# Kernel tuning notes

Hardware: AMD Instinct MI355X
Metric: run time of the kernel (lower is better)

## Reference

```python
import jax, jax.numpy as jnp
import numpy as np

D_MODEL = 2048
N_HEADS = 16
D_HEAD = 128
ROPE_BASE = 10000.0


def _rope(q, k, start_pos):
    # q, k: [B, H, S, Dh]; standard rotate-half RoPE
    S, Dh = q.shape[-2], q.shape[-1]
    inv_freq = 1.0 / (ROPE_BASE ** (jnp.arange(0, Dh, 2, dtype=jnp.float32) / Dh))  # [Dh/2]
    pos = jnp.arange(S, dtype=jnp.float32) + start_pos                              # [S]
    ang = pos[:, None] * inv_freq[None, :]                                          # [S, Dh/2]
    cos = jnp.concatenate([jnp.cos(ang), jnp.cos(ang)], axis=-1)[None, None]        # [1,1,S,Dh]
    sin = jnp.concatenate([jnp.sin(ang), jnp.sin(ang)], axis=-1)[None, None]

    def rot_half(t):
        t1, t2 = jnp.split(t, 2, axis=-1)
        return jnp.concatenate([-t2, t1], axis=-1)

    return q * cos + rot_half(q) * sin, k * cos + rot_half(k) * sin


def setup_inputs() -> dict:
    key = jax.random.key(0)
    k1, k2, k3 = jax.random.split(key, 3)
    B, S = 2, 2048
    scale_in = 1.0 / np.sqrt(D_MODEL)
    x = jax.random.normal(k1, (B, S, D_MODEL), dtype=jnp.float32)
    w_qkv = jax.random.normal(k2, (3 * D_MODEL, D_MODEL), dtype=jnp.float32) * scale_in
    w_out = jax.random.normal(k3, (D_MODEL, D_MODEL), dtype=jnp.float32) * scale_in
    return {"x": x, "w_qkv": w_qkv, "w_out": w_out, "start_pos": 0}


def reference(x, w_qkv, w_out, start_pos):
    B, S, _ = x.shape
    scale = 1.0 / np.sqrt(D_HEAD)
    qkv = jnp.einsum('bsd,ed->bse', x, w_qkv)                 # [B,S,3D]
    q, k, v = jnp.split(qkv, 3, axis=-1)
    # [B,S,D] -> [B,H,S,Dh]
    reshape = lambda t: t.reshape(B, S, N_HEADS, D_HEAD).transpose(0, 2, 1, 3)
    q, k, v = reshape(q), reshape(k), reshape(v)
    q, k = _rope(q, k, start_pos)
    scores = jnp.einsum('bhqd,bhkd->bhqk', q, k) * scale      # [B,H,S,S]
    if S > 1:
        causal = jnp.tril(jnp.ones((S, S), dtype=bool))
        scores = jnp.where(causal[None, None], scores, -jnp.inf)
    attn = jax.nn.softmax(scores, axis=-1)
    out = jnp.einsum('bhqk,bhkd->bhqd', attn, v)              # [B,H,S,Dh]
    out = out.transpose(0, 2, 1, 3).reshape(B, S, D_MODEL)
    return jnp.einsum('bsd,ed->bse', out, w_out)
```

## Files before the change

kernel.cpp:

```cpp
#include <hip/hip_runtime.h>

typedef unsigned short ushort;
typedef __attribute__((ext_vector_type(8))) short short8;
typedef __attribute__((ext_vector_type(4))) float f32x4;

#define NH 16
#define DH 128
#define SEQ 2048
#define DMODEL 2048
#define GK 2048

__device__ __forceinline__ ushort f2bf(float f) {
  union { float f; unsigned u; } v; v.f = f;
  unsigned u = v.u;
  unsigned r = (u + 0x7fffu + ((u >> 16) & 1u)) >> 16;
  return (ushort)r;
}
__device__ __forceinline__ float bf2f(ushort h) {
  union { unsigned u; float f; } v; v.u = ((unsigned)h) << 16; return v.f;
}

__device__ __forceinline__ void async16(const ushort* g, ushort* l) {
  __builtin_amdgcn_global_load_lds(
      (const __attribute__((address_space(1))) unsigned*)g,
      (__attribute__((address_space(3))) unsigned*)l, 16, 0, 0);
}

__global__ void cast_kernel(const float* __restrict__ src, ushort* __restrict__ dst, int n4) {
  int i = blockIdx.x * blockDim.x + threadIdx.x;
  if (i >= n4) return;
  float4 v = ((const float4*)src)[i];
  unsigned long long p = (unsigned long long)f2bf(v.x)
                       | ((unsigned long long)f2bf(v.y) << 16)
                       | ((unsigned long long)f2bf(v.z) << 32)
                       | ((unsigned long long)f2bf(v.w) << 48);
  ((unsigned long long*)dst)[i] = p;
}

template<int MODE>
__global__ __launch_bounds__(256, 2)
void gemm_bt(const ushort* __restrict__ A, const ushort* __restrict__ B, int N,
             ushort* __restrict__ oq, ushort* __restrict__ ok, ushort* __restrict__ ov,
             float* __restrict__ of) {
  __shared__ ushort As[128 * 64];
  __shared__ ushort Bs[128 * 64];
  const int tid = threadIdx.x;
  const int lane = tid & 63;
  const int w = tid >> 6;
  const int wr = w >> 1, wc = w & 1;
  const int g = lane >> 4, l16 = lane & 15;
  const int m0 = blockIdx.y * 128;
  const int n0 = blockIdx.x * 128;

  f32x4 acc[4][4];
#pragma unroll
  for (int i = 0; i < 4; ++i)
#pragma unroll
    for (int j = 0; j < 4; ++j) acc[i][j] = (f32x4)0.f;

  const ushort* Ablk = A + (size_t)m0 * GK;
  const ushort* Bblk = B + (size_t)n0 * GK;

  for (int k0 = 0; k0 < GK; k0 += 64) {
#pragma unroll
    for (int it = 0; it < 4; ++it) {
      int e = (it * 256 + tid) * 8;
      int row = e >> 6, col = e & 63;
      async16(Ablk + (size_t)row * GK + k0 + col, &As[e]);
      async16(Bblk + (size_t)row * GK + k0 + col, &Bs[e]);
    }
    __syncthreads();
#pragma unroll
    for (int ks = 0; ks < 2; ++ks) {
      short8 af[4], bf[4];
#pragma unroll
      for (int mf = 0; mf < 4; ++mf)
        af[mf] = *(const short8*)&As[(wr * 64 + mf * 16 + l16) * 64 + ks * 32 + g * 8];
#pragma unroll
      for (int nf = 0; nf < 4; ++nf)
        bf[nf] = *(const short8*)&Bs[(wc * 64 + nf * 16 + l16) * 64 + ks * 32 + g * 8];
#pragma unroll
      for (int mf = 0; mf < 4; ++mf)
#pragma unroll
        for (int nf = 0; nf < 4; ++nf)
          acc[mf][nf] = __builtin_amdgcn_mfma_f32_16x16x32_bf16(af[mf], bf[nf], acc[mf][nf], 0, 0, 0);
    }
    __syncthreads();
  }

#pragma unroll
  for (int mf = 0; mf < 4; ++mf)
#pragma unroll
    for (int nf = 0; nf < 4; ++nf)
#pragma unroll
      for (int i = 0; i < 4; ++i) {
        int row = m0 + wr * 64 + mf * 16 + g * 4 + i;
        int col = n0 + wc * 64 + nf * 16 + l16;
        float val = acc[mf][nf][i];
        if (MODE == 0) {
          int which = col >> 11;
          int r = col & 2047;
          int h = r >> 7, dh = r & 127;
          int b = row >> 11, s = row & 2047;
          size_t dst = ((size_t)(b * NH + h) * SEQ + s) * DH + dh;
          ushort* o = (which == 0) ? oq : (which == 1 ? ok : ov);
          o[dst] = f2bf(val);
        } else {
          of[(size_t)row * N + col] = val;
        }
      }
}

__global__ void rope_kernel(ushort* __restrict__ q, ushort* __restrict__ k,
                            const int* __restrict__ spp) {
  int id = blockIdx.x * blockDim.x + threadIdx.x;
  int j = id & 63;
  int s = (id >> 6) & (SEQ - 1);
  int bh = id >> 17;
  size_t base = ((size_t)bh * SEQ + s) * DH;
  float pos = (float)(s + spp[0]);
  float ang = pos * __expf(-(float)j * (9.210340371976184f / 64.f));
  float c = cosf(ang), sn = sinf(ang);
  float q1 = bf2f(q[base + j]), q2 = bf2f(q[base + 64 + j]);
  q[base + j]      = f2bf(q1 * c - q2 * sn);
  q[base + 64 + j] = f2bf(q2 * c + q1 * sn);
  float k1 = bf2f(k[base + j]), k2 = bf2f(k[base + 64 + j]);
  k[base + j]      = f2bf(k1 * c - k2 * sn);
  k[base + 64 + j] = f2bf(k2 * c + k1 * sn);
}

__global__ __launch_bounds__(256, 2)
void attn_kernel(const ushort* __restrict__ Q, const ushort* __restrict__ K,
                 const ushort* __restrict__ V, ushort* __restrict__ O) {
  __shared__ ushort Ks[2][64 * 128];
  __shared__ ushort Vt[2][128 * 72];
  __shared__ ushort Ps[4][16 * 72];
  const int tid = threadIdx.x;
  const int lane = tid & 63;
  const int w = tid >> 6;
  const int g = lane >> 4, l16 = lane & 15;
  const int h = blockIdx.y, b = blockIdx.z;
  const int bh = b * NH + h;
  const ushort* Qb = Q + (size_t)bh * SEQ * DH;
  const ushort* Kb = K + (size_t)bh * SEQ * DH;
  const ushort* Vb = V + (size_t)bh * SEQ * DH;
  const float scale = 0.08838834764831845f;

  const int vkv = (tid >> 3) * 2;
  const int vd0 = (tid & 7) * 16;
  const int vmask = (tid & 7) << 3;

  for (int pass = 0; pass < 2; ++pass) {
    const int qt = pass == 0 ? (31 - (int)blockIdx.x) : (int)blockIdx.x;
    const int q0 = qt * 64;
    const int nkt = qt + 1;

    short8 qf[4];
    {
      const ushort* qrow = Qb + (size_t)(q0 + w * 16 + l16) * DH;
#pragma unroll
      for (int ks = 0; ks < 4; ++ks) qf[ks] = *(const short8*)(qrow + ks * 32 + g * 8);
    }
    f32x4 oacc[8];
#pragma unroll
    for (int i = 0; i < 8; ++i) oacc[i] = (f32x4)0.f;
    float m_i[4], l_i[4];
#pragma unroll
    for (int i = 0; i < 4; ++i) { m_i[i] = -INFINITY; l_i[i] = 0.f; }

#pragma unroll
    for (int it = 0; it < 4; ++it) {
      int ci = it * 256 + tid;
      int row = ci >> 4;
      int cb = ((ci & 15) * 16) ^ ((row & 7) << 4);
      async16(Kb + (size_t)row * DH + (cb >> 1), &Ks[0][ci * 8]);
    }
    {
      short8 vr[4];
      vr[0] = *(const short8*)(Vb + (size_t)vkv * DH + vd0);
      vr[1] = *(const short8*)(Vb + (size_t)vkv * DH + vd0 + 8);
      vr[2] = *(const short8*)(Vb + (size_t)(vkv + 1) * DH + vd0);
      vr[3] = *(const short8*)(Vb + (size_t)(vkv + 1) * DH + vd0 + 8);
#pragma unroll
      for (int j = 0; j < 16; ++j) {
        int d = vd0 + j;
        const ushort* a = (const ushort*)&vr[j >> 3];
        const ushort* c = (const ushort*)&vr[2 + (j >> 3)];
        unsigned val = (unsigned)a[j & 7] | ((unsigned)c[j & 7] << 16);
        *(unsigned*)&Vt[0][d * 72 + (vkv ^ vmask)] = val;
      }
    }
    __syncthreads();

    int cur = 0;
    for (int t = 0; t < nkt; ++t) {
      const int k0 = t * 64;
      const int nxt = cur ^ 1;
      const bool pre = (t + 1 < nkt);
      short8 vr[4];
      if (pre) {
        const int kn = (t + 1) * 64;
#pragma unroll
        for (int it = 0; it < 4; ++it) {
          int ci = it * 256 + tid;
          int row = ci >> 4;
          int cb = ((ci & 15) * 16) ^ ((row & 7) << 4);
          async16(Kb + (size_t)(kn + row) * DH + (cb >> 1), &Ks[nxt][ci * 8]);
        }
        vr[0] = *(const short8*)(Vb + (size_t)(kn + vkv) * DH + vd0);
        vr[1] = *(const short8*)(Vb + (size_t)(kn + vkv) * DH + vd0 + 8);
        vr[2] = *(const short8*)(Vb + (size_t)(kn + vkv + 1) * DH + vd0);
        vr[3] = *(const short8*)(Vb + (size_t)(kn + vkv + 1) * DH + vd0 + 8);
      }

      f32x4 sacc[4];
#pragma unroll
      for (int nf = 0; nf < 4; ++nf) sacc[nf] = (f32x4)0.f;
      __builtin_amdgcn_s_setprio(1);
#pragma unroll
      for (int nf = 0; nf < 4; ++nf) {
        int row = nf * 16 + l16;
#pragma unroll
        for (int ks = 0; ks < 4; ++ks) {
          int cb = (ks * 64 + g * 16) ^ ((l16 & 7) << 4);
          short8 kf = *(const short8*)&Ks[cur][row * 128 + (cb >> 1)];
          sacc[nf] = __builtin_amdgcn_mfma_f32_16x16x32_bf16(qf[ks], kf, sacc[nf], 0, 0, 0);
        }
      }
      __builtin_amdgcn_s_setprio(0);

#pragma unroll
      for (int i = 0; i < 4; ++i) {
        int qrow = q0 + w * 16 + g * 4 + i;
        float pv[4];
#pragma unroll
        for (int nf = 0; nf < 4; ++nf) {
          pv[nf] = sacc[nf][i] * scale;
          if (k0 + nf * 16 + l16 > qrow) pv[nf] = -INFINITY;
        }
        float mx = fmaxf(fmaxf(pv[0], pv[1]), fmaxf(pv[2], pv[3]));
#pragma unroll
        for (int d = 1; d < 16; d <<= 1) mx = fmaxf(mx, __shfl_xor(mx, d, 64));
        float mnew = fmaxf(m_i[i], mx);
        float alpha = __expf(m_i[i] - mnew);
        float p[4], sum = 0.f;
#pragma unroll
        for (int nf = 0; nf < 4; ++nf) { p[nf] = __expf(pv[nf] - mnew); sum += p[nf]; }
#pragma unroll
        for (int d = 1; d < 16; d <<= 1) sum += __shfl_xor(sum, d, 64);
        l_i[i] = l_i[i] * alpha + sum;
        m_i[i] = mnew;
#pragma unroll
        for (int nf2 = 0; nf2 < 8; ++nf2) oacc[nf2][i] *= alpha;
#pragma unroll
        for (int nf = 0; nf < 4; ++nf)
          Ps[w][(g * 4 + i) * 72 + nf * 16 + l16] = f2bf(p[nf]);
      }
      __asm__ volatile("s_waitcnt lgkmcnt(0)" ::: "memory");
      __builtin_amdgcn_sched_barrier(0);

      __builtin_amdgcn_s_setprio(1);
#pragma unroll
      for (int kvh = 0; kvh < 2; ++kvh) {
        short8 pa = *(const short8*)&Ps[w][l16 * 72 + kvh * 32 + g * 8];
#pragma unroll
        for (int nf2 = 0; nf2 < 8; ++nf2) {
          int cb = (kvh * 32 + g * 8) ^ (nf2 * 8);
          short8 vf = *(const short8*)&Vt[cur][(nf2 * 16 + l16) * 72 + cb];
          oacc[nf2] = __builtin_amdgcn_mfma_f32_16x16x32_bf16(pa, vf, oacc[nf2], 0, 0, 0);
        }
      }
      __builtin_amdgcn_s_setprio(0);

      if (pre) {
#pragma unroll
        for (int j = 0; j < 16; ++j) {
          int d = vd0 + j;
          const ushort* a = (const ushort*)&vr[j >> 3];
          const ushort* c = (const ushort*)&vr[2 + (j >> 3)];
          unsigned val = (unsigned)a[j & 7] | ((unsigned)c[j & 7] << 16);
          *(unsigned*)&Vt[nxt][d * 72 + (vkv ^ vmask)] = val;
        }
      }
      __syncthreads();
      cur = nxt;
    }

#pragma unroll
    for (int i = 0; i < 4; ++i) {
      float inv = 1.f / l_i[i];
      int row = q0 + w * 16 + g * 4 + i;
      size_t obase = ((size_t)b * SEQ + row) * DMODEL + h * DH;
#pragma unroll
      for (int nf2 = 0; nf2 < 8; ++nf2)
        O[obase + nf2 * 16 + l16] = f2bf(oacc[nf2][i] * inv);
    }
  }
}

extern "C" void kernel_launch(void* const* d_in, const int* in_sizes, int n_in,
                              void* d_out, int out_size, void* d_ws, size_t ws_size,
                              hipStream_t stream) {
  const float* x    = (const float*)d_in[0];
  const float* wqkv = (const float*)d_in[1];
  const float* wout = (const float*)d_in[2];
  const int*   spp  = (const int*)d_in[3];
  float* out = (float*)d_out;

  ushort* ws = (ushort*)d_ws;
  ushort* xb  = ws;
  ushort* wqb = xb + 8388608;
  ushort* wob = wqb + 12582912;
  ushort* q   = wob + 4194304;
  ushort* k   = q + 8388608;
  ushort* v   = k + 8388608;
  ushort* ao  = v + 8388608;

  cast_kernel<<<8388608 / 1024, 256, 0, stream>>>(x, xb, 8388608 / 4);
  cast_kernel<<<12582912 / 1024, 256, 0, stream>>>(wqkv, wqb, 12582912 / 4);
  cast_kernel<<<4194304 / 1024, 256, 0, stream>>>(wout, wob, 4194304 / 4);

  gemm_bt<0><<<dim3(6144 / 128, 4096 / 128), 256, 0, stream>>>(xb, wqb, 6144, q, k, v, nullptr);

  rope_kernel<<<4194304 / 256, 256, 0, stream>>>(q, k, spp);

  attn_kernel<<<dim3(16, NH, 2), 256, 0, stream>>>(q, k, v, ao);

  gemm_bt<1><<<dim3(2048 / 128, 4096 / 128), 256, 0, stream>>>(ao, wob, 2048, nullptr, nullptr, nullptr, out);
}
```

Baseline: 300.1 us.

## Replace GEMM with 256x256-tile double-buffered pipelined kernel with swizzled LDS

```diff
diff --git a/kernel.cpp b/kernel.cpp
--- a/kernel.cpp
+++ b/kernel.cpp
@@ -9,6 +9,9 @@
 #define SEQ 2048
 #define DMODEL 2048
 #define GK 2048
+#define NT 32
+
+#define WAITVM(N) asm volatile("s_waitcnt vmcnt(" #N ")" ::: "memory")
 
 __device__ __forceinline__ ushort f2bf(float f) {
   union { float f; unsigned u; } v; v.f = f;
@@ -37,65 +40,115 @@
   ((unsigned long long*)dst)[i] = p;
 }
 
+__device__ __forceinline__ void stageA(const ushort* Ablk, int k0, ushort* dst, int half, int tid) {
+#pragma unroll
+  for (int j = 0; j < 2; ++j) {
+    int c = j * 512 + tid;
+    int rl = c >> 3, slot = c & 7;
+    int grow = half * 128 + rl;
+    int col = ((slot * 16) ^ ((rl & 7) << 4)) >> 1;
+    async16(Ablk + (size_t)grow * GK + k0 + col, dst + half * 8192 + c * 8);
+  }
+}
+__device__ __forceinline__ void stageB2(const ushort* Bblk, int k0, ushort* dst, int pair, int tid) {
+#pragma unroll
+  for (int j = 0; j < 2; ++j) {
+    int u = pair * 2 + j;
+    int grow = u * 64 + (tid >> 3);
+    int slot = tid & 7;
+    int col = ((slot * 16) ^ ((grow & 7) << 4)) >> 1;
+    async16(Bblk + (size_t)grow * GK + k0 + col, dst + u * 4096 + tid * 8);
+  }
+}
+
 template<int MODE>
-__global__ __launch_bounds__(256, 2)
-void gemm_bt(const ushort* __restrict__ A, const ushort* __restrict__ B, int N,
+__global__ __launch_bounds__(512, 1)
+void gemm256(const ushort* __restrict__ A, const ushort* __restrict__ B, int N,
              ushort* __restrict__ oq, ushort* __restrict__ ok, ushort* __restrict__ ov,
              float* __restrict__ of) {
-  __shared__ ushort As[128 * 64];
-  __shared__ ushort Bs[128 * 64];
+  __shared__ ushort As[2 * 256 * 64];
+  __shared__ ushort Bs[2 * 256 * 64];
   const int tid = threadIdx.x;
   const int lane = tid & 63;
   const int w = tid >> 6;
-  const int wr = w >> 1, wc = w & 1;
   const int g = lane >> 4, l16 = lane & 15;
-  const int m0 = blockIdx.y * 128;
-  const int n0 = blockIdx.x * 128;
-
-  f32x4 acc[4][4];
-#pragma unroll
-  for (int i = 0; i < 4; ++i)
-#pragma unroll
-    for (int j = 0; j < 4; ++j) acc[i][j] = (f32x4)0.f;
-
+  const int m0 = blockIdx.y * 256;
+  const int n0 = blockIdx.x * 256;
   const ushort* Ablk = A + (size_t)m0 * GK;
   const ushort* Bblk = B + (size_t)n0 * GK;
 
-  for (int k0 = 0; k0 < GK; k0 += 64) {
-#pragma unroll
-    for (int it = 0; it < 4; ++it) {
-      int e = (it * 256 + tid) * 8;
-      int row = e >> 6, col = e & 63;
-      async16(Ablk + (size_t)row * GK + k0 + col, &As[e]);
-      async16(Bblk + (size_t)row * GK + k0 + col, &Bs[e]);
-    }
-    __syncthreads();
-#pragma unroll
-    for (int ks = 0; ks < 2; ++ks) {
-      short8 af[4], bf[4];
-#pragma unroll
-      for (int mf = 0; mf < 4; ++mf)
-        af[mf] = *(const short8*)&As[(wr * 64 + mf * 16 + l16) * 64 + ks * 32 + g * 8];
-#pragma unroll
-      for (int nf = 0; nf < 4; ++nf)
-        bf[nf] = *(const short8*)&Bs[(wc * 64 + nf * 16 + l16) * 64 + ks * 32 + g * 8];
-#pragma unroll
-      for (int mf = 0; mf < 4; ++mf)
-#pragma unroll
-        for (int nf = 0; nf < 4; ++nf)
-          acc[mf][nf] = __builtin_amdgcn_mfma_f32_16x16x32_bf16(af[mf], bf[nf], acc[mf][nf], 0, 0, 0);
-    }
-    __syncthreads();
+  f32x4 acc[2][16];
+#pragma unroll
+  for (int mf = 0; mf < 2; ++mf)
+#pragma unroll
+    for (int nf = 0; nf < 16; ++nf) acc[mf][nf] = (f32x4)0.f;
+
+  stageA(Ablk, 0, As, 0, tid);
+  stageA(Ablk, 0, As, 1, tid);
+  stageB2(Bblk, 0, Bs, 0, tid);
+  stageB2(Bblk, 0, Bs, 1, tid);
+
+  for (int t = 0; t < NT; ++t) {
+    const int kn = (t + 1) * 64;
+    const bool pre = (t + 1 < NT);
+    ushort* curA = As + (t & 1) * 16384;
+    ushort* curB = Bs + (t & 1) * 16384;
+    ushort* nxtA = As + ((t & 1) ^ 1) * 16384;
+    ushort* nxtB = Bs + ((t & 1) ^ 1) * 16384;
+    short8 af[2][2];
+#pragma unroll
+    for (int p = 0; p < 4; ++p) {
+      if (pre) {
+        if (p == 0)      stageA(Ablk, kn, nxtA, 0, tid);
+        else if (p == 1) stageA(Ablk, kn, nxtA, 1, tid);
+        else if (p == 2) stageB2(Bblk, kn, nxtB, 0, tid);
+        else             stageB2(Bblk, kn, nxtB, 1, tid);
+        if (p == 0) { WAITVM(5); } else if (p == 1) { WAITVM(6); }
+        else if (p == 2) { WAITVM(7); } else { WAITVM(8); }
+      } else {
+        if (p == 0) { WAITVM(3); } else if (p == 1) { WAITVM(2); }
+        else if (p == 2) { WAITVM(1); } else { WAITVM(0); }
+      }
+      __builtin_amdgcn_sched_barrier(0);
+      __builtin_amdgcn_s_barrier();
+      if (p == 0) {
+#pragma unroll
+        for (int mf = 0; mf < 2; ++mf)
+#pragma unroll
+          for (int ks = 0; ks < 2; ++ks) {
+            int row = w * 32 + mf * 16 + l16;
+            af[mf][ks] = *(const short8*)&curA[row * 64 + (((ks * 64 + g * 16) ^ ((l16 & 7) << 4)) >> 1)];
+          }
+      }
+      short8 bfr[4][2];
+#pragma unroll
+      for (int nfi = 0; nfi < 4; ++nfi)
+#pragma unroll
+        for (int ks = 0; ks < 2; ++ks) {
+          int row = (p * 4 + nfi) * 16 + l16;
+          bfr[nfi][ks] = *(const short8*)&curB[row * 64 + (((ks * 64 + g * 16) ^ ((l16 & 7) << 4)) >> 1)];
+        }
+      __builtin_amdgcn_s_setprio(1);
+#pragma unroll
+      for (int nfi = 0; nfi < 4; ++nfi)
+#pragma unroll
+        for (int mf = 0; mf < 2; ++mf)
+#pragma unroll
+          for (int ks = 0; ks < 2; ++ks)
+            acc[mf][p * 4 + nfi] = __builtin_amdgcn_mfma_f32_16x16x32_bf16(
+                af[mf][ks], bfr[nfi][ks], acc[mf][p * 4 + nfi], 0, 0, 0);
+      __builtin_amdgcn_s_setprio(0);
+    }
   }
 
 #pragma unroll
-  for (int mf = 0; mf < 4; ++mf)
-#pragma unroll
-    for (int nf = 0; nf < 4; ++nf)
+  for (int mf = 0; mf < 2; ++mf)
+#pragma unroll
+    for (int nf = 0; nf < 16; ++nf)
 #pragma unroll
       for (int i = 0; i < 4; ++i) {
-        int row = m0 + wr * 64 + mf * 16 + g * 4 + i;
-        int col = n0 + wc * 64 + nf * 16 + l16;
+        int row = m0 + w * 32 + mf * 16 + g * 4 + i;
+        int col = n0 + nf * 16 + l16;
         float val = acc[mf][nf][i];
         if (MODE == 0) {
           int which = col >> 11;
@@ -320,11 +373,11 @@
   cast_kernel<<<12582912 / 1024, 256, 0, stream>>>(wqkv, wqb, 12582912 / 4);
   cast_kernel<<<4194304 / 1024, 256, 0, stream>>>(wout, wob, 4194304 / 4);
 
-  gemm_bt<0><<<dim3(6144 / 128, 4096 / 128), 256, 0, stream>>>(xb, wqb, 6144, q, k, v, nullptr);
+  gemm256<0><<<dim3(6144 / 256, 4096 / 256), 512, 0, stream>>>(xb, wqb, 6144, q, k, v, nullptr);
 
   rope_kernel<<<4194304 / 256, 256, 0, stream>>>(q, k, spp);
 
   attn_kernel<<<dim3(16, NH, 2), 256, 0, stream>>>(q, k, v, ao);
 
-  gemm_bt<1><<<dim3(2048 / 128, 4096 / 128), 256, 0, stream>>>(ao, wob, 2048, nullptr, nullptr, nullptr, out);
-}
+  gemm256<1><<<dim3(2048 / 256, 4096 / 256), 512, 0, stream>>>(ao, wob, 2048, nullptr, nullptr, nullptr, out);
+}
```

New measurement: 309.0 us. 1.03x slower.

## Double-buffer GEMM with 128x256 tiles, swizzled LDS and interleaved prefetch

Applied to the files above, without the earlier changes.

```diff
diff --git a/kernel.cpp b/kernel.cpp
--- a/kernel.cpp
+++ b/kernel.cpp
@@ -9,6 +9,9 @@
 #define SEQ 2048
 #define DMODEL 2048
 #define GK 2048
+#define NT 32
+
+#define WAITVM(N) asm volatile("s_waitcnt vmcnt(" #N ")" ::: "memory")
 
 __device__ __forceinline__ ushort f2bf(float f) {
   union { float f; unsigned u; } v; v.f = f;
@@ -37,55 +40,100 @@
   ((unsigned long long*)dst)[i] = p;
 }
 
+__device__ __forceinline__ void stageA128(const ushort* Ablk, int k0, ushort* dst,
+                                          int half, int tid) {
+  int rl = tid >> 3, slot = tid & 7;
+  int grow = half * 64 + rl;
+  int col = ((slot * 16) ^ ((grow & 7) << 4)) >> 1;
+  async16(Ablk + (size_t)grow * GK + k0 + col, dst + half * 4096 + tid * 8);
+}
+__device__ __forceinline__ void stageB256(const ushort* Bblk, int k0, ushort* dst,
+                                          int pair, int tid) {
+#pragma unroll
+  for (int j = 0; j < 2; ++j) {
+    int u = pair * 2 + j;
+    int grow = u * 64 + (tid >> 3);
+    int slot = tid & 7;
+    int col = ((slot * 16) ^ ((grow & 7) << 4)) >> 1;
+    async16(Bblk + (size_t)grow * GK + k0 + col, dst + u * 4096 + tid * 8);
+  }
+}
+
 template<int MODE>
-__global__ __launch_bounds__(256, 2)
-void gemm_bt(const ushort* __restrict__ A, const ushort* __restrict__ B, int N,
+__global__ __launch_bounds__(512, 1)
+void gemm128(const ushort* __restrict__ A, const ushort* __restrict__ B, int N,
              ushort* __restrict__ oq, ushort* __restrict__ ok, ushort* __restrict__ ov,
              float* __restrict__ of) {
-  __shared__ ushort As[128 * 64];
-  __shared__ ushort Bs[128 * 64];
+  __shared__ ushort As[2][128 * 64];
+  __shared__ ushort Bs[2][256 * 64];
   const int tid = threadIdx.x;
   const int lane = tid & 63;
   const int w = tid >> 6;
-  const int wr = w >> 1, wc = w & 1;
+  const int wr = w >> 2, wc = w & 3;
   const int g = lane >> 4, l16 = lane & 15;
   const int m0 = blockIdx.y * 128;
-  const int n0 = blockIdx.x * 128;
-
-  f32x4 acc[4][4];
-#pragma unroll
-  for (int i = 0; i < 4; ++i)
-#pragma unroll
-    for (int j = 0; j < 4; ++j) acc[i][j] = (f32x4)0.f;
-
+  const int n0 = blockIdx.x * 256;
   const ushort* Ablk = A + (size_t)m0 * GK;
   const ushort* Bblk = B + (size_t)n0 * GK;
 
-  for (int k0 = 0; k0 < GK; k0 += 64) {
-#pragma unroll
-    for (int it = 0; it < 4; ++it) {
-      int e = (it * 256 + tid) * 8;
-      int row = e >> 6, col = e & 63;
-      async16(Ablk + (size_t)row * GK + k0 + col, &As[e]);
-      async16(Bblk + (size_t)row * GK + k0 + col, &Bs[e]);
-    }
-    __syncthreads();
-#pragma unroll
-    for (int ks = 0; ks < 2; ++ks) {
-      short8 af[4], bf[4];
-#pragma unroll
-      for (int mf = 0; mf < 4; ++mf)
-        af[mf] = *(const short8*)&As[(wr * 64 + mf * 16 + l16) * 64 + ks * 32 + g * 8];
+  f32x4 acc[4][4];
+#pragma unroll
+  for (int mf = 0; mf < 4; ++mf)
+#pragma unroll
+    for (int nf = 0; nf < 4; ++nf) acc[mf][nf] = (f32x4)0.f;
+
+  stageA128(Ablk, 0, As[0], 0, tid);
+  stageA128(Ablk, 0, As[0], 1, tid);
+  stageB256(Bblk, 0, Bs[0], 0, tid);
+  stageB256(Bblk, 0, Bs[0], 1, tid);
+
+  for (int t = 0; t < NT; ++t) {
+    const int kn = (t + 1) * 64;
+    const bool pre = (t + 1 < NT);
+    const ushort* curA = As[t & 1];
+    const ushort* curB = Bs[t & 1];
+    ushort* nxtA = (ushort*)As[(t & 1) ^ 1];
+    ushort* nxtB = (ushort*)Bs[(t & 1) ^ 1];
+
+    if (pre) { stageA128(Ablk, kn, nxtA, 0, tid); WAITVM(1); }
+    else     { WAITVM(0); }
+    __builtin_amdgcn_sched_barrier(0);
+    __builtin_amdgcn_s_barrier();
+    __builtin_amdgcn_sched_barrier(0);
+
+    short8 bfr[4][2];
+#pragma unroll
+    for (int nf = 0; nf < 4; ++nf)
+#pragma unroll
+      for (int ks = 0; ks < 2; ++ks) {
+        int row = wc * 64 + nf * 16 + l16;
+        bfr[nf][ks] = *(const short8*)&curB[row * 64 + (((ks * 64 + g * 16) ^ ((l16 & 7) << 4)) >> 1)];
+      }
+
+#pragma unroll
+    for (int p = 0; p < 4; ++p) {
+      if (pre) {
+        if (p == 1)      stageA128(Ablk, kn, nxtA, 1, tid);
+        else if (p == 2) stageB256(Bblk, kn, nxtB, 0, tid);
+        else if (p == 3) stageB256(Bblk, kn, nxtB, 1, tid);
+      }
+      short8 af[2];
+      int row = wr * 64 + p * 16 + l16;
+#pragma unroll
+      for (int ks = 0; ks < 2; ++ks)
+        af[ks] = *(const short8*)&curA[row * 64 + (((ks * 64 + g * 16) ^ ((l16 & 7) << 4)) >> 1)];
+      __builtin_amdgcn_s_setprio(1);
 #pragma unroll
       for (int nf = 0; nf < 4; ++nf)
-        bf[nf] = *(const short8*)&Bs[(wc * 64 + nf * 16 + l16) * 64 + ks * 32 + g * 8];
-#pragma unroll
-      for (int mf = 0; mf < 4; ++mf)
-#pragma unroll
-        for (int nf = 0; nf < 4; ++nf)
-          acc[mf][nf] = __builtin_amdgcn_mfma_f32_16x16x32_bf16(af[mf], bf[nf], acc[mf][nf], 0, 0, 0);
-    }
-    __syncthreads();
+#pragma unroll
+        for (int ks = 0; ks < 2; ++ks)
+          acc[p][nf] = __builtin_amdgcn_mfma_f32_16x16x32_bf16(af[ks], bfr[nf][ks], acc[p][nf], 0, 0, 0);
+      __builtin_amdgcn_s_setprio(0);
+    }
+
+    __builtin_amdgcn_sched_barrier(0);
+    __builtin_amdgcn_s_barrier();
+    __builtin_amdgcn_sched_barrier(0);
   }
 
 #pragma unroll
@@ -320,11 +368,11 @@
   cast_kernel<<<12582912 / 1024, 256, 0, stream>>>(wqkv, wqb, 12582912 / 4);
   cast_kernel<<<4194304 / 1024, 256, 0, stream>>>(wout, wob, 4194304 / 4);
 
-  gemm_bt<0><<<dim3(6144 / 128, 4096 / 128), 256, 0, stream>>>(xb, wqb, 6144, q, k, v, nullptr);
+  gemm128<0><<<dim3(6144 / 256, 4096 / 128), 512, 0, stream>>>(xb, wqb, 6144, q, k, v, nullptr);
 
   rope_kernel<<<4194304 / 256, 256, 0, stream>>>(q, k, spp);
 
   attn_kernel<<<dim3(16, NH, 2), 256, 0, stream>>>(q, k, v, ao);
 
-  gemm_bt<1><<<dim3(2048 / 128, 4096 / 128), 256, 0, stream>>>(ao, wob, 2048, nullptr, nullptr, nullptr, out);
-}
+  gemm128<1><<<dim3(2048 / 256, 4096 / 128), 512, 0, stream>>>(ao, wob, 2048, nullptr, nullptr, nullptr, out);
+}
```

Measured after the change: 317.7 us. 5.8% more time.
